# Optimization experiments

Measured on AMD Instinct MI355X. Metric: run time of the kernel, lower is better.

The kernel has to match this reference:

```python
import jax, jax.numpy as jnp
import numpy as np

NUM_CLUSTERS = 512


def setup_inputs() -> dict:
    key = jax.random.key(0)
    k1, k2 = jax.random.split(key)
    N, F, K = 131072, 64, NUM_CLUSTERS
    z_e = jax.random.normal(k1, (N, F), dtype=jnp.float32)
    # torch init: uniform(-1/K, 1/K) for embedding weight [F, K]
    W = jax.random.uniform(k2, (F, K), dtype=jnp.float32, minval=-1.0 / K, maxval=1.0 / K)
    return {"z_e": z_e, "W": W}


def reference(z_e, W):
    # squared-distance matrix [N, K] via expansion: ||z||^2 - 2 z.W + ||w||^2
    distances = (
        jnp.sum(z_e * z_e, axis=1, keepdims=True)
        - 2.0 * (z_e @ W)
        + jnp.sum(W * W, axis=0, keepdims=True)
    )
    encoding_idx = jnp.argmin(distances, axis=-1)  # [N]
    encodings = jax.nn.one_hot(encoding_idx, NUM_CLUSTERS, dtype=z_e.dtype)  # [N, K]
    z_q = jnp.take(W, encoding_idx, axis=1).T  # gather == encodings @ W.T, [N, F]
    diff = (jax.lax.stop_gradient(z_q) - z_e) ** 2
    z_q = z_e + jax.lax.stop_gradient(z_q - z_e)  # straight-through
    return z_q, encoding_idx[:, None], encodings, diff
```

## Files before the change

### kernel.cpp

```cpp
#include <hip/hip_runtime.h>

#define K_CLUSTERS 512
#define FDIM 64
#define RPB 512
#define RT 8
#define NTILES 4
#define WSTRIDE 17

typedef float vf4 __attribute__((ext_vector_type(4)));

__global__ __launch_bounds__(64) void vq_prep(const float* __restrict__ W,
                                              float* __restrict__ Wt,
                                              float* __restrict__ wsq) {
    int k = blockIdx.x;
    int f = threadIdx.x;
    float w = W[f * K_CLUSTERS + k];
    Wt[k * FDIM + f] = w;
    float s = w * w;
#pragma unroll
    for (int off = 32; off > 0; off >>= 1) s += __shfl_xor(s, off, 64);
    if (f == 0) wsq[k] = s;
}

__global__ __launch_bounds__(1024)
__attribute__((amdgpu_waves_per_eu(4, 4)))
void vq_fused(const float* __restrict__ z,
              const float* __restrict__ W,
              const float* __restrict__ Wt,
              const float* __restrict__ wsq,
              float* __restrict__ out_zq,
              float* __restrict__ out_idx,
              float* __restrict__ enc,
              float* __restrict__ out_diff) {
    __shared__ vf4 sW4[K_CLUSTERS * WSTRIDE];

    const int tid = threadIdx.x;
    const int w = __builtin_amdgcn_readfirstlane(tid) >> 6;
    const int l = tid & 63;

    {
        float* sWf = (float*)sW4;
        const vf4* Wg4 = (const vf4*)W;
#pragma unroll
        for (int it = 0; it < 8; it++) {
            int u4 = it * 1024 + tid;
            vf4 v = Wg4[u4];
            int u = u4 << 2;
            int f = u >> 9;
            int c0 = u & 511;
            int f4 = f >> 2, m = f & 3;
#pragma unroll
            for (int e = 0; e < 4; e++) {
                int c = c0 + e;
                sWf[c * (4 * WSTRIDE) + (f4 << 2) + m] = v[e];
            }
        }
    }
    __syncthreads();

    const int rowW = blockIdx.x * RPB + w * (RT * NTILES);
    const vf4* zg4 = (const vf4*)z;
    const vf4* wB = sW4 + l * WSTRIDE;
    const vf4* wB4 = wB + 256 * WSTRIDE;

#pragma unroll 1
    for (int t = 0; t < NTILES; t++) {
        const int row0 = rowW + t * RT;

        float srow;
        {
            const float* zr = z + (size_t)(row0 + (l >> 3)) * FDIM;
            const int j = l & 7;
            float rj;
            {
#pragma clang fp contract(off)
                rj = zr[j] * zr[j];
#pragma unroll
                for (int b = 8; b < 64; b += 8) rj += zr[b + j] * zr[b + j];
            }
            float s01 = rj + __shfl_xor(rj, 1, 64);
            float s03 = s01 + __shfl_xor(s01, 2, 64);
            srow = s03 + __shfl_xor(s03, 4, 64);
        }
        float sA[RT];
#pragma unroll
        for (int r = 0; r < RT; r++) sA[r] = __shfl(srow, r << 3, 64);

        const vf4* zt = zg4 + (size_t)row0 * 16;

        float acc[RT][8];
#pragma unroll
        for (int r = 0; r < RT; r++)
#pragma unroll
            for (int j = 0; j < 8; j++) acc[r][j] = 0.0f;

#pragma unroll 1
        for (int f4 = 0; f4 < 16; f4++) {
            vf4 wv0 = wB[f4];
            vf4 wv1 = wB[64 * WSTRIDE + f4];
            vf4 wv2 = wB[128 * WSTRIDE + f4];
            vf4 wv3 = wB[192 * WSTRIDE + f4];
            vf4 wv4 = wB4[f4];
            vf4 wv5 = wB4[64 * WSTRIDE + f4];
            vf4 wv6 = wB4[128 * WSTRIDE + f4];
            vf4 wv7 = wB4[192 * WSTRIDE + f4];
#pragma unroll
            for (int r = 0; r < RT; r++) {
                vf4 zb = zt[(r << 4) + f4];
                float a0 = acc[r][0], a1 = acc[r][1], a2 = acc[r][2], a3 = acc[r][3];
                float a4 = acc[r][4], a5 = acc[r][5], a6 = acc[r][6], a7 = acc[r][7];
                a0 = fmaf(zb.x, wv0.x, a0); a1 = fmaf(zb.x, wv1.x, a1);
                a2 = fmaf(zb.x, wv2.x, a2); a3 = fmaf(zb.x, wv3.x, a3);
                a4 = fmaf(zb.x, wv4.x, a4); a5 = fmaf(zb.x, wv5.x, a5);
                a6 = fmaf(zb.x, wv6.x, a6); a7 = fmaf(zb.x, wv7.x, a7);
                a0 = fmaf(zb.y, wv0.y, a0); a1 = fmaf(zb.y, wv1.y, a1);
                a2 = fmaf(zb.y, wv2.y, a2); a3 = fmaf(zb.y, wv3.y, a3);
                a4 = fmaf(zb.y, wv4.y, a4); a5 = fmaf(zb.y, wv5.y, a5);
                a6 = fmaf(zb.y, wv6.y, a6); a7 = fmaf(zb.y, wv7.y, a7);
                a0 = fmaf(zb.z, wv0.z, a0); a1 = fmaf(zb.z, wv1.z, a1);
                a2 = fmaf(zb.z, wv2.z, a2); a3 = fmaf(zb.z, wv3.z, a3);
                a4 = fmaf(zb.z, wv4.z, a4); a5 = fmaf(zb.z, wv5.z, a5);
                a6 = fmaf(zb.z, wv6.z, a6); a7 = fmaf(zb.z, wv7.z, a7);
                a0 = fmaf(zb.w, wv0.w, a0); a1 = fmaf(zb.w, wv1.w, a1);
                a2 = fmaf(zb.w, wv2.w, a2); a3 = fmaf(zb.w, wv3.w, a3);
                a4 = fmaf(zb.w, wv4.w, a4); a5 = fmaf(zb.w, wv5.w, a5);
                a6 = fmaf(zb.w, wv6.w, a6); a7 = fmaf(zb.w, wv7.w, a7);
                acc[r][0] = a0; acc[r][1] = a1; acc[r][2] = a2; acc[r][3] = a3;
                acc[r][4] = a4; acc[r][5] = a5; acc[r][6] = a6; acc[r][7] = a7;
            }
        }

        float bd[RT];
        int bk[RT];
#pragma unroll
        for (int r = 0; r < RT; r++) { bd[r] = INFINITY; bk[r] = 0; }
#pragma unroll
        for (int j = 0; j < 8; j++) {
            const int c = (j << 6) + l;
            const float q = wsq[c];
#pragma unroll
            for (int r = 0; r < RT; r++) {
                float d = fmaf(-2.0f, acc[r][j], sA[r]) + q;
                if (d < bd[r] || (d == bd[r] && c < bk[r])) { bd[r] = d; bk[r] = c; }
            }
        }

#pragma unroll
        for (int off = 1; off < 64; off <<= 1) {
#pragma unroll
            for (int r = 0; r < RT; r++) {
                float od = __shfl_xor(bd[r], off, 64);
                int ok = __shfl_xor(bk[r], off, 64);
                if (od < bd[r] || (od == bd[r] && ok < bk[r])) { bd[r] = od; bk[r] = ok; }
            }
        }

        if (l == 0) {
#pragma unroll
            for (int r = 0; r < RT; r++) out_idx[row0 + r] = (float)bk[r];
        }

#pragma unroll
        for (int h = 0; h < 2; h++) {
            const int rsel = l >> 4;
            int kk = bk[4 * h + 0];
            if (rsel == 1) kk = bk[4 * h + 1];
            if (rsel == 2) kk = bk[4 * h + 2];
            if (rsel == 3) kk = bk[4 * h + 3];
            vf4 zvv = zt[(h << 6) + l];
            vf4 wvv = ((const vf4*)Wt)[((size_t)kk << 4) + (l & 15)];
            vf4 zq, df;
            {
#pragma clang fp contract(off)
                vf4 d1 = wvv - zvv;
                zq = zvv + d1;
                df = d1 * d1;
            }
            ((vf4*)out_zq)[(size_t)row0 * 16 + (h << 6) + l] = zq;
            ((vf4*)out_diff)[(size_t)row0 * 16 + (h << 6) + l] = df;
        }

        {
            vf4* enc4 = (vf4*)enc + (size_t)row0 * 128;
#pragma unroll
            for (int jj = 0; jj < 16; jj++) {
                const int row = jj >> 1;
                int kk = bk[row];
                int c = kk - ((l + ((jj & 1) << 6)) << 2);
                vf4 v;
                v.x = (c == 0) ? 1.0f : 0.0f;
                v.y = (c == 1) ? 1.0f : 0.0f;
                v.z = (c == 2) ? 1.0f : 0.0f;
                v.w = (c == 3) ? 1.0f : 0.0f;
                enc4[(jj << 6) + l] = v;
            }
        }
    }
}

extern "C" void kernel_launch(void* const* d_in, const int* in_sizes, int n_in,
                              void* d_out, int out_size, void* d_ws, size_t ws_size,
                              hipStream_t stream) {
    const float* z = (const float*)d_in[0];
    const float* W = (const float*)d_in[1];
    int N = in_sizes[0] / FDIM;

    float* out = (float*)d_out;
    float* out_zq = out;
    float* out_idx = out_zq + (size_t)N * FDIM;
    float* enc = out_idx + N;
    float* out_diff = enc + (size_t)N * K_CLUSTERS;

    float* Wt = (float*)d_ws;
    float* wsq = Wt + K_CLUSTERS * FDIM;

    vq_prep<<<K_CLUSTERS, 64, 0, stream>>>(W, Wt, wsq);
    vq_fused<<<N / RPB, 1024, 0, stream>>>(z, W, Wt, wsq, out_zq, out_idx, enc, out_diff);
}
```

Baseline: 449.5 us.

## Split fused VQ kernel into argmin kernel and separate epilogue kernel

Splits the fused kernel in two. The first kernel computes only the distances and the argmin and writes the indices. A new lightweight kernel then reads the indices back, gathers codebook rows, and writes z_q, diff and the one-hot encodings. The aim is to move the write-heavy epilogue, dominated by the 256MB one-hot output, out of the low-occupancy, LDS-heavy compute kernel so that many more waves can drive the stores. The cost is an extra launch, z being read a second time, and the index round trip through memory.

```diff
diff --git a/kernel.cpp b/kernel.cpp
--- a/kernel.cpp
+++ b/kernel.cpp
@@ -24,14 +24,10 @@
 
 __global__ __launch_bounds__(1024)
 __attribute__((amdgpu_waves_per_eu(4, 4)))
-void vq_fused(const float* __restrict__ z,
-              const float* __restrict__ W,
-              const float* __restrict__ Wt,
-              const float* __restrict__ wsq,
-              float* __restrict__ out_zq,
-              float* __restrict__ out_idx,
-              float* __restrict__ enc,
-              float* __restrict__ out_diff) {
+void vq_argmin(const float* __restrict__ z,
+               const float* __restrict__ W,
+               const float* __restrict__ wsq,
+               float* __restrict__ out_idx) {
     __shared__ vf4 sW4[K_CLUSTERS * WSTRIDE];
 
     const int tid = threadIdx.x;
@@ -159,41 +155,62 @@
 #pragma unroll
             for (int r = 0; r < RT; r++) out_idx[row0 + r] = (float)bk[r];
         }
-
-#pragma unroll
-        for (int h = 0; h < 2; h++) {
-            const int rsel = l >> 4;
-            int kk = bk[4 * h + 0];
-            if (rsel == 1) kk = bk[4 * h + 1];
-            if (rsel == 2) kk = bk[4 * h + 2];
-            if (rsel == 3) kk = bk[4 * h + 3];
-            vf4 zvv = zt[(h << 6) + l];
-            vf4 wvv = ((const vf4*)Wt)[((size_t)kk << 4) + (l & 15)];
-            vf4 zq, df;
-            {
+    }
+}
+
+__global__ __launch_bounds__(256) void vq_epi(const float* __restrict__ z,
+                                              const float* __restrict__ Wt,
+                                              const float* __restrict__ idxf,
+                                              float* __restrict__ out_zq,
+                                              float* __restrict__ enc,
+                                              float* __restrict__ out_diff) {
+    const int tid = threadIdx.x;
+    const int w = __builtin_amdgcn_readfirstlane(tid) >> 6;
+    const int l = tid & 63;
+    const int row0 = blockIdx.x * 16 + (w << 2);
+
+    const int bk0 = (int)idxf[row0 + 0];
+    const int bk1 = (int)idxf[row0 + 1];
+    const int bk2 = (int)idxf[row0 + 2];
+    const int bk3 = (int)idxf[row0 + 3];
+
+    const vf4* zt = (const vf4*)z + (size_t)row0 * 16;
+
+    {
+        const int rsel = l >> 4;
+        int kk = bk0;
+        if (rsel == 1) kk = bk1;
+        if (rsel == 2) kk = bk2;
+        if (rsel == 3) kk = bk3;
+        vf4 zvv = zt[l];
+        vf4 wvv = ((const vf4*)Wt)[((size_t)kk << 4) + (l & 15)];
+        vf4 zq, df;
+        {
 #pragma clang fp contract(off)
-                vf4 d1 = wvv - zvv;
-                zq = zvv + d1;
-                df = d1 * d1;
-            }
-            ((vf4*)out_zq)[(size_t)row0 * 16 + (h << 6) + l] = zq;
-            ((vf4*)out_diff)[(size_t)row0 * 16 + (h << 6) + l] = df;
-        }
-
-        {
-            vf4* enc4 = (vf4*)enc + (size_t)row0 * 128;
-#pragma unroll
-            for (int jj = 0; jj < 16; jj++) {
-                const int row = jj >> 1;
-                int kk = bk[row];
-                int c = kk - ((l + ((jj & 1) << 6)) << 2);
-                vf4 v;
-                v.x = (c == 0) ? 1.0f : 0.0f;
-                v.y = (c == 1) ? 1.0f : 0.0f;
-                v.z = (c == 2) ? 1.0f : 0.0f;
-                v.w = (c == 3) ? 1.0f : 0.0f;
-                enc4[(jj << 6) + l] = v;
-            }
+            vf4 d1 = wvv - zvv;
+            zq = zvv + d1;
+            df = d1 * d1;
+        }
+        ((vf4*)out_zq)[(size_t)row0 * 16 + l] = zq;
+        ((vf4*)out_diff)[(size_t)row0 * 16 + l] = df;
+    }
+
+    {
+        vf4* enc4 = (vf4*)enc + (size_t)row0 * 128;
+#pragma unroll
+        for (int jj = 0; jj < 8; jj++) {
+            const int row = jj >> 1;
+            int kk = bk0;
+            if (row == 1) kk = bk1;
+            if (row == 2) kk = bk2;
+            if (row == 3) kk = bk3;
+            int c = kk - ((l + ((jj & 1) << 6)) << 2);
+            vf4 v;
+            v.x = (c == 0) ? 1.0f : 0.0f;
+            v.y = (c == 1) ? 1.0f : 0.0f;
+            v.z = (c == 2) ? 1.0f : 0.0f;
+            v.w = (c == 3) ? 1.0f : 0.0f;
+            enc4[(jj << 6) + l] = v;
         }
     }
 }
@@ -215,5 +232,6 @@
     float* wsq = Wt + K_CLUSTERS * FDIM;
 
     vq_prep<<<K_CLUSTERS, 64, 0, stream>>>(W, Wt, wsq);
-    vq_fused<<<N / RPB, 1024, 0, stream>>>(z, W, Wt, wsq, out_zq, out_idx, enc, out_diff);
-}
+    vq_argmin<<<N / RPB, 1024, 0, stream>>>(z, W, wsq, out_idx);
+    vq_epi<<<N / 16, 256, 0, stream>>>(z, Wt, out_idx, out_zq, enc, out_diff);
+}
```

Result: slower. 473.9 us (+5.4%).
